# Optimization experiments

Measured on AMD Instinct MI355X. Metric: run time of the kernel, lower is better.

Reference implementation:

```python
import jax, jax.numpy as jnp
import numpy as np

B = 4096
C = 32000

def setup_inputs() -> dict:
    key = jax.random.key(0)
    k1, k2 = jax.random.split(key)
    output = jax.random.normal(k1, (B, C), dtype=jnp.float32)
    target = jax.random.randint(k2, (B,), 0, C, dtype=jnp.int64)
    return {"output": output, "target": target}

def reference(output, target):
    # probs: [B, C]
    probs = jax.nn.softmax(output, axis=1)
    batch_size, num_classes = probs.shape
    avg_conf = jnp.mean(probs, axis=0)  # [C]
    # avg_count[c] = mean(target == c)  == bincount(target)/B, fused scatter-add
    counts = jnp.zeros((num_classes,), dtype=probs.dtype).at[target].add(1.0)
    avg_count = counts / batch_size
    loss_mdca = jnp.mean(jnp.abs(avg_conf - avg_count))
    return loss_mdca
```

## Files before the change

### kernel.cpp

```cpp
#include <hip/hip_runtime.h>

#define BB 4096
#define CC 32000
#define CPAD 32768
#define NT 1024
#define NI 8
#define GRID 256
#define RPB (BB / GRID)
#define NW (NT / 64)
#define FBLK (CPAD / 4 / 256)

typedef float v4f __attribute__((ext_vector_type(4)));

__global__ __launch_bounds__(NT, 4) void mdca_main(const float* __restrict__ x,
                                                   const int* __restrict__ tgt,
                                                   float* __restrict__ partial,
                                                   float* __restrict__ counts) {
    __shared__ float red[2][NW];

    const int t = threadIdx.x;
    const int wid = t >> 6;
    const int r0 = blockIdx.x * RPB;

    const bool tail_ok = ((NI - 1) * (NT * 4) + 4 * t) < CC;

    v4f cur[NI], nxt[NI], acc[NI];
#pragma unroll
    for (int i = 0; i < NI; ++i) acc[i] = (v4f){0.f, 0.f, 0.f, 0.f};

    {
        const float* rp = x + (size_t)r0 * CC;
#pragma unroll
        for (int i = 0; i < NI; ++i) {
            const int col = i * (NT * 4) + 4 * t;
            if (i < NI - 1 || tail_ok) cur[i] = *(const v4f*)(rp + col);
        }
    }

    for (int r = 0; r < RPB; ++r) {
        const int p = r & 1;
        if (r + 1 < RPB) {
            const float* rq = x + (size_t)(r0 + r + 1) * CC;
#pragma unroll
            for (int i = 0; i < NI; ++i) {
                const int col = i * (NT * 4) + 4 * t;
                if (i < NI - 1 || tail_ok) nxt[i] = *(const v4f*)(rq + col);
            }
        }
        float s = 0.f;
#pragma unroll
        for (int i = 0; i < NI; ++i) {
            if (i < NI - 1 || tail_ok) {
                v4f e;
                e.x = __expf(cur[i].x); e.y = __expf(cur[i].y);
                e.z = __expf(cur[i].z); e.w = __expf(cur[i].w);
                cur[i] = e;
                s += e.x + e.y + e.z + e.w;
            }
        }
        for (int off = 32; off > 0; off >>= 1) s += __shfl_down(s, off);
        if ((t & 63) == 0) red[p][wid] = s;
        __syncthreads();
        float z = 0.f;
#pragma unroll
        for (int w = 0; w < NW; ++w) z += red[p][w];
        const float rz = 1.0f / z;
#pragma unroll
        for (int i = 0; i < NI; ++i) {
            if (i < NI - 1 || tail_ok) {
                acc[i].x += cur[i].x * rz; acc[i].y += cur[i].y * rz;
                acc[i].z += cur[i].z * rz; acc[i].w += cur[i].w * rz;
            }
        }
        if (r + 1 < RPB) {
#pragma unroll
            for (int i = 0; i < NI; ++i) cur[i] = nxt[i];
        }
    }

    v4f* pp = (v4f*)(partial + (size_t)blockIdx.x * CPAD);
#pragma unroll
    for (int i = 0; i < NI; ++i) pp[i * NT + t] = acc[i];

    if (t < RPB) atomicAdd(&counts[tgt[r0 + t]], 1.0f);
}

__global__ __launch_bounds__(256) void finalize(const float* __restrict__ partial,
                                                const float* __restrict__ counts,
                                                float* __restrict__ total,
                                                unsigned* __restrict__ blkcnt,
                                                float* __restrict__ out) {
    const int g = blockIdx.x * 256 + threadIdx.x;
    v4f s = {0.f, 0.f, 0.f, 0.f};
    const v4f* pv = (const v4f*)partial;
#pragma unroll 4
    for (int b = 0; b < GRID; ++b) {
        v4f p = pv[(size_t)b * (CPAD / 4) + g];
        s.x += p.x; s.y += p.y; s.z += p.z; s.w += p.w;
    }
    float v = 0.f;
    const int c = 4 * g;
    if (c < CC) {
        v4f cnt = *(const v4f*)(counts + c);
        v = fabsf(s.x - cnt.x) + fabsf(s.y - cnt.y) + fabsf(s.z - cnt.z) + fabsf(s.w - cnt.w);
    }
    for (int off = 32; off > 0; off >>= 1) v += __shfl_down(v, off);
    __shared__ float wsum[4];
    if ((threadIdx.x & 63) == 0) wsum[threadIdx.x >> 6] = v;
    __syncthreads();
    if (threadIdx.x == 0) {
        atomicAdd(total, wsum[0] + wsum[1] + wsum[2] + wsum[3]);
        __threadfence();
        unsigned prev = atomicAdd(blkcnt, 1u);
        if (prev == FBLK - 1) {
            float tot = atomicAdd(total, 0.0f);
            out[0] = tot * (1.0f / ((float)BB * (float)CC));
        }
    }
}

extern "C" void kernel_launch(void* const* d_in, const int* in_sizes, int n_in,
                              void* d_out, int out_size, void* d_ws, size_t ws_size,
                              hipStream_t stream) {
    const float* x = (const float*)d_in[0];
    const int* tgt = (const int*)d_in[1];
    float* out = (float*)d_out;

    float* partial = (float*)d_ws;
    float* counts = partial + (size_t)GRID * CPAD;
    float* total = counts + CC;
    unsigned* blkcnt = (unsigned*)(total + 1);

    (void)hipMemsetAsync(counts, 0, (size_t)(CC + 2) * 4, stream);

    mdca_main<<<GRID, NT, 0, stream>>>(x, tgt, partial, counts);
    finalize<<<FBLK, 256, 0, stream>>>(partial, counts, total, blkcnt, out);
}
```

Measured before the change: 688.7 us.

## Split fused softmax-mean into row-normalizer pass and column-accumulate pass

Replaces the single fused kernel, where each 1024-thread block handles 16 rows while holding them in registers, with two passes. The first computes each row's reciprocal softmax denominator with one block per row. The second reads the input again and accumulates exp(x)*rcpZ over row slabs per column block, which exposes far more blocks and cuts register pressure. The cost is reading the 524MB input twice and computing exp twice, in exchange for better occupancy and fewer partial rows for finalize to reduce.

```diff
diff --git a/kernel.cpp b/kernel.cpp
--- a/kernel.cpp
+++ b/kernel.cpp
@@ -3,86 +3,74 @@
 #define BB 4096
 #define CC 32000
 #define CPAD 32768
-#define NT 1024
-#define NI 8
-#define GRID 256
-#define RPB (BB / GRID)
-#define NW (NT / 64)
+#define QR (CC / 4)
+
+#define NT1 256
+#define NIT1 ((QR + NT1 - 1) / NT1)
+
+#define NT2 512
+#define NCB (CPAD / (NT2 * 4))
+#define NRB 128
+#define RSLAB (BB / NRB)
+#define NP NRB
+
 #define FBLK (CPAD / 4 / 256)
 
 typedef float v4f __attribute__((ext_vector_type(4)));
 
-__global__ __launch_bounds__(NT, 4) void mdca_main(const float* __restrict__ x,
-                                                   const int* __restrict__ tgt,
-                                                   float* __restrict__ partial,
-                                                   float* __restrict__ counts) {
-    __shared__ float red[2][NW];
+__global__ __launch_bounds__(NT1) void pass1_z(const float* __restrict__ x,
+                                               const int* __restrict__ tgt,
+                                               float* __restrict__ rcpZ,
+                                               float* __restrict__ counts) {
+    const int t = threadIdx.x;
+    const int r = blockIdx.x;
+    const float* rp = x + (size_t)r * CC;
 
-    const int t = threadIdx.x;
-    const int wid = t >> 6;
-    const int r0 = blockIdx.x * RPB;
-
-    const bool tail_ok = ((NI - 1) * (NT * 4) + 4 * t) < CC;
-
-    v4f cur[NI], nxt[NI], acc[NI];
-#pragma unroll
-    for (int i = 0; i < NI; ++i) acc[i] = (v4f){0.f, 0.f, 0.f, 0.f};
-
-    {
-        const float* rp = x + (size_t)r0 * CC;
-#pragma unroll
-        for (int i = 0; i < NI; ++i) {
-            const int col = i * (NT * 4) + 4 * t;
-            if (i < NI - 1 || tail_ok) cur[i] = *(const v4f*)(rp + col);
+    float s = 0.f;
+#pragma unroll 4
+    for (int i = 0; i < NIT1; ++i) {
+        const int q = i * NT1 + t;
+        if (q < QR) {
+            v4f v = *(const v4f*)(rp + 4 * q);
+            s += __expf(v.x) + __expf(v.y) + __expf(v.z) + __expf(v.w);
         }
     }
-
-    for (int r = 0; r < RPB; ++r) {
-        const int p = r & 1;
-        if (r + 1 < RPB) {
-            const float* rq = x + (size_t)(r0 + r + 1) * CC;
-#pragma unroll
-            for (int i = 0; i < NI; ++i) {
-                const int col = i * (NT * 4) + 4 * t;
-                if (i < NI - 1 || tail_ok) nxt[i] = *(const v4f*)(rq + col);
-            }
-        }
-        float s = 0.f;
-#pragma unroll
-        for (int i = 0; i < NI; ++i) {
-            if (i < NI - 1 || tail_ok) {
-                v4f e;
-                e.x = __expf(cur[i].x); e.y = __expf(cur[i].y);
-                e.z = __expf(cur[i].z); e.w = __expf(cur[i].w);
-                cur[i] = e;
-                s += e.x + e.y + e.z + e.w;
-            }
-        }
-        for (int off = 32; off > 0; off >>= 1) s += __shfl_down(s, off);
-        if ((t & 63) == 0) red[p][wid] = s;
-        __syncthreads();
+    for (int off = 32; off > 0; off >>= 1) s += __shfl_down(s, off);
+    __shared__ float red[NT1 / 64];
+    if ((t & 63) == 0) red[t >> 6] = s;
+    __syncthreads();
+    if (t == 0) {
         float z = 0.f;
 #pragma unroll
-        for (int w = 0; w < NW; ++w) z += red[p][w];
-        const float rz = 1.0f / z;
-#pragma unroll
-        for (int i = 0; i < NI; ++i) {
-            if (i < NI - 1 || tail_ok) {
-                acc[i].x += cur[i].x * rz; acc[i].y += cur[i].y * rz;
-                acc[i].z += cur[i].z * rz; acc[i].w += cur[i].w * rz;
-            }
-        }
-        if (r + 1 < RPB) {
-#pragma unroll
-            for (int i = 0; i < NI; ++i) cur[i] = nxt[i];
+        for (int w = 0; w < NT1 / 64; ++w) z += red[w];
+        rcpZ[r] = 1.0f / z;
+        atomicAdd(&counts[tgt[r]], 1.0f);
+    }
+}
+
+__global__ __launch_bounds__(NT2) void pass2_acc(const float* __restrict__ x,
+                                                 const float* __restrict__ rcpZ,
+                                                 float* __restrict__ partial) {
+    const int t = threadIdx.x;
+    const int cb = blockIdx.x & (NCB - 1);
+    const int rb = blockIdx.x / NCB;
+    const int col = cb * (NT2 * 4) + 4 * t;
+    const int r0 = rb * RSLAB;
+
+    v4f acc = {0.f, 0.f, 0.f, 0.f};
+    if (col < CC) {
+        const float* p = x + (size_t)r0 * CC + col;
+#pragma unroll 8
+        for (int r = 0; r < RSLAB; ++r) {
+            v4f v = *(const v4f*)(p + (size_t)r * CC);
+            const float rz = rcpZ[r0 + r];
+            acc.x += __expf(v.x) * rz;
+            acc.y += __expf(v.y) * rz;
+            acc.z += __expf(v.z) * rz;
+            acc.w += __expf(v.w) * rz;
         }
     }
-
-    v4f* pp = (v4f*)(partial + (size_t)blockIdx.x * CPAD);
-#pragma unroll
-    for (int i = 0; i < NI; ++i) pp[i * NT + t] = acc[i];
-
-    if (t < RPB) atomicAdd(&counts[tgt[r0 + t]], 1.0f);
+    *(v4f*)(partial + (size_t)rb * CPAD + col) = acc;
 }
 
 __global__ __launch_bounds__(256) void finalize(const float* __restrict__ partial,
@@ -94,7 +82,7 @@
     v4f s = {0.f, 0.f, 0.f, 0.f};
     const v4f* pv = (const v4f*)partial;
 #pragma unroll 4
-    for (int b = 0; b < GRID; ++b) {
+    for (int b = 0; b < NP; ++b) {
         v4f p = pv[(size_t)b * (CPAD / 4) + g];
         s.x += p.x; s.y += p.y; s.z += p.z; s.w += p.w;
     }
@@ -127,12 +115,14 @@
     float* out = (float*)d_out;
 
     float* partial = (float*)d_ws;
-    float* counts = partial + (size_t)GRID * CPAD;
+    float* counts = partial + (size_t)NP * CPAD;
     float* total = counts + CC;
     unsigned* blkcnt = (unsigned*)(total + 1);
+    float* rcpZ = (float*)(blkcnt + 1);
 
     (void)hipMemsetAsync(counts, 0, (size_t)(CC + 2) * 4, stream);
 
-    mdca_main<<<GRID, NT, 0, stream>>>(x, tgt, partial, counts);
+    pass1_z<<<BB, NT1, 0, stream>>>(x, tgt, rcpZ, counts);
+    pass2_acc<<<NCB * NRB, NT2, 0, stream>>>(x, rcpZ, partial);
     finalize<<<FBLK, 256, 0, stream>>>(partial, counts, total, blkcnt, out);
 }
```

New measurement: 779.7 us. 1.13x slower.
